# Kernel tuning notes

Hardware: AMD Instinct MI355X
Metric: run time of the kernel (lower is better)

Reference implementation:

```python
import jax, jax.numpy as jnp
import numpy as np

B, C, CI, H, W = 8, 1024, 512, 56, 56
BN_EPS = 1e-5


def _conv1x1(x, w, b):
    # x: [B,C,H,W], w: [O,C], b: [O] -> [B,O,H,W]
    return jnp.einsum('bchw,oc->bohw', x, w) + b[None, :, None, None]


def setup_inputs() -> dict:
    key = jax.random.key(0)
    ks = jax.random.split(key, 12)
    s = lambda k, shape: (jax.random.normal(k, shape, jnp.float32) * 0.02)
    return {
        'x': jax.random.normal(ks[0], (B, C, H, W), jnp.float32),
        'theta_w': s(ks[1], (CI, C)), 'theta_b': s(ks[2], (CI,)),
        'phi_w': s(ks[3], (CI, C)), 'phi_b': s(ks[4], (CI,)),
        'g_w': s(ks[5], (CI, C)), 'g_b': s(ks[6], (CI,)),
        'wz_w': s(ks[7], (C, CI)), 'wz_b': s(ks[8], (C,)),
        'bn_gamma': 1.0 + 0.1 * jax.random.normal(ks[9], (C,), jnp.float32),
        'bn_beta': s(ks[10], (C,)),
    }


def reference(x, theta_w, theta_b, phi_w, phi_b, g_w, g_b, wz_w, wz_b, bn_gamma, bn_beta):
    b, c, h, w = x.shape
    n = h * w
    # 1x1-conv projections, flattened to token sequences
    g_x = _conv1x1(x, g_w, g_b).reshape(b, -1, n).transpose(0, 2, 1)       # [B,N,CI]
    theta_x = _conv1x1(x, theta_w, theta_b).reshape(b, -1, n).transpose(0, 2, 1)  # [B,N,CI]
    phi_x = _conv1x1(x, phi_w, phi_b).reshape(b, -1, n)                     # [B,CI,N]
    # embedded-gaussian: f = theta @ phi^T, softmax over last dim
    f = jnp.einsum('bnc,bcm->bnm', theta_x, phi_x)                          # [B,N,N]
    attn = jax.nn.softmax(f, axis=-1)
    y = jnp.einsum('bnm,bmc->bnc', attn, g_x)                               # [B,N,CI]
    y = y.transpose(0, 2, 1).reshape(b, -1, h, w)                           # [B,CI,H,W]
    z = _conv1x1(y, wz_w, wz_b)                                             # [B,C,H,W]
    # BatchNorm2d in training mode: batch statistics over (B,H,W), biased var
    mean = z.mean(axis=(0, 2, 3))
    var = z.var(axis=(0, 2, 3))
    zn = (z - mean[None, :, None, None]) * jax.lax.rsqrt(var + BN_EPS)[None, :, None, None]
    zn = zn * bn_gamma[None, :, None, None] + bn_beta[None, :, None, None]
    return zn + x
```

## Files before the change

### kernel.cpp

```cpp
#include <hip/hip_runtime.h>
#include <cstdint>
#include <cstdio>

#define DEVINL __device__ __forceinline__

typedef _Float16 f16x8 __attribute__((ext_vector_type(8)));
typedef float    f32x4 __attribute__((ext_vector_type(4)));

static constexpr int B_  = 8;
static constexpr int C_  = 1024;
static constexpr int CI_ = 512;
static constexpr int N_  = 56 * 56;
static constexpr int NP  = 3328;
static constexpr float BN_EPS = 1e-5f;

DEVINL uint16_t f2h(float f) {
  union { _Float16 h; uint16_t u; } cv;
  cv.h = (_Float16)f;
  return cv.u;
}

DEVINL void async16(const void* g, void* lds) {
  __builtin_amdgcn_global_load_lds(
      (const __attribute__((address_space(1))) uint32_t*)g,
      (__attribute__((address_space(3))) uint32_t*)lds, 16, 0, 0);
}

template <int BIAS>
__global__ __launch_bounds__(512, 2) void gemm256(
    const uint16_t* __restrict__ A, const uint16_t* __restrict__ Bt,
    uint16_t* __restrict__ Cc, const float* __restrict__ bias,
    int K, int lda, int ldb, int ldc,
    long aBatch, long bBatch, long cBatch, int nbx, int nby) {
  __shared__ uint16_t lds[65536];

  const int nwg = gridDim.x, orig = blockIdx.x;
  const int q = nwg >> 3, r = nwg & 7, xcd = orig & 7, idx = orig >> 3;
  const int wgid = (xcd < r ? xcd * (q + 1) : r * (q + 1) + (xcd - r) * q) + idx;
  const int bx = wgid % nbx;
  const int by = (wgid / nbx) % nby;
  const int zb = wgid / (nbx * nby);

  const int tid = threadIdx.x, w = tid >> 6, l = tid & 63;
  const int wm = w >> 2, wn = w & 3, lr = l & 15, lg = l >> 4;

  const uint16_t* Ab = A + (long)zb * aBatch + (long)bx * 256 * lda;
  const uint16_t* Bb = Bt + (long)zb * bBatch + (long)by * 256 * ldb;

  const int NT = K >> 6;

  const int c0 = tid, c1 = 512 + tid;
  const long aoff0 = (long)(c0 >> 2) * lda + (((c0 & 3) ^ ((c0 >> 3) & 3)) * 8);
  const long aoff1 = (long)(c1 >> 2) * lda + (((c1 & 3) ^ ((c1 >> 3) & 3)) * 8);
  const long boff0 = (long)(c0 >> 2) * ldb + (((c0 & 3) ^ ((c0 >> 3) & 3)) * 8);
  const long boff1 = (long)(c1 >> 2) * ldb + (((c1 & 3) ^ ((c1 >> 3) & 3)) * 8);
  const int ldsW0 = (w * 64) * 8;
  const int ldsW1 = (512 + w * 64) * 8;

  auto stageA = [&](int t, int ks, int buf) {
    const int tw = t >= NT ? t - NT : t;
    const uint16_t* src = Ab + tw * 64 + ks * 32;
    const int reg = (buf * 2 + ks) * 8192;
    async16(src + aoff0, &lds[reg + ldsW0]);
    async16(src + aoff1, &lds[reg + ldsW1]);
  };
  auto stageB = [&](int t, int ks, int buf) {
    const int tw = t >= NT ? t - NT : t;
    const uint16_t* src = Bb + tw * 64 + ks * 32;
    const int reg = 32768 + (buf * 2 + ks) * 8192;
    async16(src + boff0, &lds[reg + ldsW0]);
    async16(src + boff1, &lds[reg + ldsW1]);
  };

  const int laneSwz = (lg ^ ((lr >> 1) & 3)) * 8;
  f32x4 acc[8][4] = {};
  f16x8 af[4], bf[4];

#define LOAD_A(b, ks, mh)                                                     \
  _Pragma("unroll") for (int i = 0; i < 4; ++i) {                             \
    const int row_ = wm * 128 + ((mh) * 4 + i) * 16 + lr;                     \
    af[i] = *reinterpret_cast<const f16x8*>(                                  \
        &lds[((b) * 2 + (ks)) * 8192 + row_ * 32 + laneSwz]);                 \
  }
#define LOAD_B(b, ks)                                                         \
  _Pragma("unroll") for (int i = 0; i < 4; ++i) {                             \
    const int row_ = wn * 64 + i * 16 + lr;                                   \
    bf[i] = *reinterpret_cast<const f16x8*>(                                  \
        &lds[32768 + ((b) * 2 + (ks)) * 8192 + row_ * 32 + laneSwz]);         \
  }
#define MFMA16(mh)                                                            \
  _Pragma("unroll") for (int i = 0; i < 4; ++i)                               \
  _Pragma("unroll") for (int j = 0; j < 4; ++j)                               \
    acc[(mh) * 4 + i][j] = __builtin_amdgcn_mfma_f32_16x16x32_f16(            \
        af[i], bf[j], acc[(mh) * 4 + i][j], 0, 0, 0);
#define WAIT_LGKM()                                       \
  asm volatile("s_waitcnt lgkmcnt(0)" ::: "memory");      \
  __builtin_amdgcn_sched_barrier(0);
#define WAIT_VM8()                                        \
  asm volatile("s_waitcnt vmcnt(8)" ::: "memory");        \
  __builtin_amdgcn_sched_barrier(0);

#define TILE(t, b)                                                            \
  {                                                                           \
                                                   \
    LOAD_B(b, 0); LOAD_A(b, 0, 0);                                            \
    stageA((t) + 1, 1, (b) ^ 1);                                              \
    __builtin_amdgcn_s_barrier(); WAIT_LGKM();                                \
    __builtin_amdgcn_s_setprio(1); MFMA16(0); __builtin_amdgcn_s_setprio(0);  \
    __builtin_amdgcn_s_barrier();                                             \
                                                   \
    LOAD_A(b, 0, 1);                                                          \
    stageB((t) + 1, 1, (b) ^ 1);                                              \
    __builtin_amdgcn_s_barrier(); WAIT_LGKM();                                \
    __builtin_amdgcn_s_setprio(1); MFMA16(1); __builtin_amdgcn_s_setprio(0);  \
    WAIT_VM8();                                                               \
    __builtin_amdgcn_s_barrier();                                             \
                                                   \
    LOAD_B(b, 1); LOAD_A(b, 1, 0);                                            \
    stageA((t) + 2, 0, (b));                                                  \
    __builtin_amdgcn_s_barrier(); WAIT_LGKM();                                \
    __builtin_amdgcn_s_setprio(1); MFMA16(0); __builtin_amdgcn_s_setprio(0);  \
    __builtin_amdgcn_s_barrier();                                             \
                                                   \
    LOAD_A(b, 1, 1);                                                          \
    stageB((t) + 2, 0, (b));                                                  \
    __builtin_amdgcn_s_barrier(); WAIT_LGKM();                                \
    __builtin_amdgcn_s_setprio(1); MFMA16(1); __builtin_amdgcn_s_setprio(0);  \
    WAIT_VM8();                                                               \
    __builtin_amdgcn_s_barrier();                                             \
  }

  stageA(0, 0, 0); stageB(0, 0, 0);
  stageA(0, 1, 0); stageB(0, 1, 0);
  stageA(1, 0, 1); stageB(1, 0, 1);
  WAIT_VM8();
  __builtin_amdgcn_s_barrier();

  for (int tp = 0; tp < NT; tp += 2) {
    TILE(tp, 0);
    TILE(tp + 1, 1);
  }

#undef TILE
#undef LOAD_A
#undef LOAD_B
#undef MFMA16
#undef WAIT_LGKM
#undef WAIT_VM8

  uint16_t* Cp = Cc + (long)zb * cBatch + ((long)bx * 256) * ldc + (long)by * 256;
#pragma unroll
  for (int mf = 0; mf < 8; ++mf) {
#pragma unroll
    for (int nf = 0; nf < 4; ++nf) {
      const int col = wn * 64 + nf * 16 + lr;
      const f32x4 v = acc[mf][nf];
#pragma unroll
      for (int qq = 0; qq < 4; ++qq) {
        const int row = wm * 128 + mf * 16 + lg * 4 + qq;
        float val = v[qq];
        if constexpr (BIAS == 1) val += bias[bx * 256 + row];
        if constexpr (BIAS == 2) val += bias[by * 256 + col];
        Cp[(long)row * ldc + col] = f2h(val);
      }
    }
  }
}

__global__ __launch_bounds__(256) void transpose_cast(
    const float* __restrict__ x, uint16_t* __restrict__ xT) {
  __shared__ float t[32][33];
  const int b = blockIdx.z;
  const float* xb = x + (long)b * C_ * N_;
  uint16_t* xTb = xT + (long)b * NP * C_;
  const int n0 = blockIdx.x * 32, c0 = blockIdx.y * 32;
  const int tx = threadIdx.x & 31, ty = threadIdx.x >> 5;
#pragma unroll
  for (int i = 0; i < 4; ++i) {
    const int cc = c0 + ty + i * 8, nn = n0 + tx;
    t[ty + i * 8][tx] = (nn < N_) ? xb[(long)cc * N_ + nn] : 0.f;
  }
  __syncthreads();
#pragma unroll
  for (int i = 0; i < 4; ++i) {
    const int nn = n0 + ty + i * 8, cc = c0 + tx;
    xTb[(long)nn * C_ + cc] = f2h(t[tx][ty + i * 8]);
  }
}

__global__ __launch_bounds__(256) void cvt_f16(
    const float* __restrict__ src, uint16_t* __restrict__ dst, int n) {
  int i = blockIdx.x * 256 + threadIdx.x;
  const int stride = gridDim.x * 256;
  for (; i < n; i += stride) dst[i] = f2h(src[i]);
}

__global__ __launch_bounds__(256) void concat_bias(
    const float* __restrict__ a, const float* __restrict__ b,
    float* __restrict__ d) {
  const int i = blockIdx.x * 256 + threadIdx.x;
  if (i < 512) d[i] = a[i];
  else if (i < 1024) d[i] = b[i - 512];
}

__global__ __launch_bounds__(256) void softmax_inplace(uint16_t* __restrict__ f) {
  const int row = blockIdx.x, tid = threadIdx.x;
  uint16_t* p = f + ((long)blockIdx.y * NP + row) * NP;
  if (row >= N_) {
    for (int i = tid; i < NP; i += 256) p[i] = 0;
    return;
  }
  __shared__ float buf[N_];
  __shared__ float red[8];
  float mx = -3.4e38f;
  for (int ch = tid; ch < N_ / 8; ch += 256) {
    const f16x8 v = *reinterpret_cast<const f16x8*>(p + ch * 8);
#pragma unroll
    for (int j = 0; j < 8; ++j) {
      const float fv = (float)v[j];
      buf[ch * 8 + j] = fv;
      mx = fmaxf(mx, fv);
    }
  }
  for (int o = 32; o; o >>= 1) mx = fmaxf(mx, __shfl_xor(mx, o));
  if ((tid & 63) == 0) red[tid >> 6] = mx;
  __syncthreads();
  mx = fmaxf(fmaxf(red[0], red[1]), fmaxf(red[2], red[3]));

  float s = 0.f;
  for (int i = tid; i < N_; i += 256) {
    const float e = __expf(buf[i] - mx);
    buf[i] = e;
    s += e;
  }
  for (int o = 32; o; o >>= 1) s += __shfl_xor(s, o);
  __syncthreads();
  if ((tid & 63) == 0) red[tid >> 6] = s;
  __syncthreads();
  const float rinv = 1.0f / (red[0] + red[1] + red[2] + red[3]);

  for (int ch = tid; ch < N_ / 8; ch += 256) {
    f16x8 o8;
#pragma unroll
    for (int j = 0; j < 8; ++j) o8[j] = (_Float16)(buf[ch * 8 + j] * rinv);
    *reinterpret_cast<f16x8*>(p + ch * 8) = o8;
  }
  for (int i = N_ + tid; i < NP; i += 256) p[i] = 0;
}

__global__ __launch_bounds__(256) void bn_stats(
    const _Float16* __restrict__ z, const float* __restrict__ gamma,
    const float* __restrict__ beta, float* __restrict__ ss) {
  const int c = blockIdx.x, tid = threadIdx.x;
  float sum = 0.f, sq = 0.f;
  for (int b = 0; b < B_; ++b) {
    const _Float16* zp = z + ((long)b * C_ + c) * NP;
    for (int ch = tid; ch < N_ / 8; ch += 256) {
      const f16x8 v = *(const f16x8*)(zp + ch * 8);
#pragma unroll
      for (int j = 0; j < 8; ++j) {
        const float fv = (float)v[j];
        sum += fv;
        sq += fv * fv;
      }
    }
  }
  for (int o = 32; o; o >>= 1) {
    sum += __shfl_xor(sum, o);
    sq += __shfl_xor(sq, o);
  }
  __shared__ float r1[8], r2[8];
  if ((tid & 63) == 0) { r1[tid >> 6] = sum; r2[tid >> 6] = sq; }
  __syncthreads();
  if (tid == 0) {
    sum = r1[0] + r1[1] + r1[2] + r1[3];
    sq  = r2[0] + r2[1] + r2[2] + r2[3];
    const float inv_n = 1.0f / (float)(B_ * N_);
    const float mean = sum * inv_n;
    const float var = sq * inv_n - mean * mean;
    const float sc = gamma[c] * rsqrtf(var + BN_EPS);
    ss[c] = sc;
    ss[C_ + c] = beta[c] - mean * sc;
  }
}

__global__ __launch_bounds__(256) void bn_apply(
    const _Float16* __restrict__ z, const float* __restrict__ x,
    const float* __restrict__ ss, float* __restrict__ out) {
  constexpr int CH = N_ / 8;
  const long nv = (long)B_ * C_ * CH;
  const long stride = (long)gridDim.x * 256;
  for (long v = (long)blockIdx.x * 256 + threadIdx.x; v < nv; v += stride) {
    const long row = v / CH;
    const int ch = (int)(v % CH);
    const int c = (int)(row % C_);
    const f16x8 zz = *(const f16x8*)(z + row * NP + ch * 8);
    const float4 x0 = *(const float4*)(x + row * (long)N_ + ch * 8);
    const float4 x1 = *(const float4*)(x + row * (long)N_ + ch * 8 + 4);
    const float sc = ss[c], sh = ss[C_ + c];
    float4 o0, o1;
    o0.x = (float)zz[0] * sc + sh + x0.x;
    o0.y = (float)zz[1] * sc + sh + x0.y;
    o0.z = (float)zz[2] * sc + sh + x0.z;
    o0.w = (float)zz[3] * sc + sh + x0.w;
    o1.x = (float)zz[4] * sc + sh + x1.x;
    o1.y = (float)zz[5] * sc + sh + x1.y;
    o1.z = (float)zz[6] * sc + sh + x1.z;
    o1.w = (float)zz[7] * sc + sh + x1.w;
    *(float4*)(out + row * (long)N_ + ch * 8) = o0;
    *(float4*)(out + row * (long)N_ + ch * 8 + 4) = o1;
  }
}

extern "C" void kernel_launch(void* const* d_in, const int* in_sizes, int n_in,
                              void* d_out, int out_size, void* d_ws,
                              size_t ws_size, hipStream_t stream) {
  const float* x       = (const float*)d_in[0];
  const float* theta_w = (const float*)d_in[1];
  const float* theta_b = (const float*)d_in[2];
  const float* phi_w   = (const float*)d_in[3];
  const float* phi_b   = (const float*)d_in[4];
  const float* g_w     = (const float*)d_in[5];
  const float* g_b     = (const float*)d_in[6];
  const float* wz_w    = (const float*)d_in[7];
  const float* wz_b    = (const float*)d_in[8];
  const float* gamma   = (const float*)d_in[9];
  const float* beta    = (const float*)d_in[10];
  float* out = (float*)d_out;

  char* ws = (char*)d_ws;
  size_t off = 0;
  auto alloc = [&](size_t bytes) {
    void* p = ws + off;
    off += (bytes + 255) & ~(size_t)255;
    return p;
  };
  uint16_t* wfused = (uint16_t*)alloc((size_t)1024 * 1024 * 2);
  uint16_t* wg     = (uint16_t*)alloc((size_t)CI_ * C_ * 2);
  uint16_t* wzh    = (uint16_t*)alloc((size_t)C_ * CI_ * 2);
  float*    bfused = (float*)alloc((size_t)1024 * 4);
  uint16_t* projT  = (uint16_t*)alloc((size_t)B_ * NP * 1024 * 2);
  uint16_t* gbuf   = (uint16_t*)alloc((size_t)B_ * CI_ * NP * 2);
  uint16_t* ybuf   = (uint16_t*)alloc((size_t)B_ * NP * CI_ * 2);
  uint16_t* zbuf   = (uint16_t*)alloc((size_t)B_ * C_ * NP * 2);
  float*    ss     = (float*)alloc((size_t)C_ * 2 * 4);

  const size_t xTb = (size_t)B_ * NP * C_ * 2;
  const size_t attnB = (size_t)NP * NP * 2;
  int G = 8;
  while (G > 1 && off + ((xTb > (size_t)G * attnB ? xTb : (size_t)G * attnB) + 255) > ws_size)
    G >>= 1;
  const size_t regionB = xTb > (size_t)G * attnB ? xTb : (size_t)G * attnB;
  uint16_t* xT    = (uint16_t*)alloc(regionB);
  uint16_t* fattn = xT;
  if (off > ws_size) {
    fprintf(stderr, "kernel_launch: workspace too small: need %zu have %zu\n",
            off, ws_size);
    return;
  }

  cvt_f16<<<512, 256, 0, stream>>>(theta_w, wfused, CI_ * C_);
  cvt_f16<<<512, 256, 0, stream>>>(phi_w, wfused + 512 * 1024, CI_ * C_);
  cvt_f16<<<512, 256, 0, stream>>>(g_w, wg, CI_ * C_);
  cvt_f16<<<512, 256, 0, stream>>>(wz_w, wzh, C_ * CI_);
  concat_bias<<<4, 256, 0, stream>>>(theta_b, phi_b, bfused);

  transpose_cast<<<dim3(NP / 32, C_ / 32, B_), 256, 0, stream>>>(x, xT);

  gemm256<2><<<dim3(B_ * NP / 256 * 4), 512, 0, stream>>>(
      xT, wfused, projT, bfused, C_, C_, C_, 1024,
      0, 0, 0, B_ * NP / 256, 4);
  gemm256<1><<<dim3(2 * 13 * B_), 512, 0, stream>>>(
      wg, xT, gbuf, g_b, C_, C_, C_, NP,
      0, (long)NP * C_, (long)CI_ * NP, 2, 13);

  for (int g0 = 0; g0 < B_; g0 += G) {
    gemm256<0><<<dim3(13 * 13 * G), 512, 0, stream>>>(
        projT + (size_t)g0 * NP * 1024, projT + (size_t)g0 * NP * 1024 + 512,
        fattn, nullptr, CI_, 1024, 1024, NP,
        (long)NP * 1024, (long)NP * 1024, (long)NP * NP, 13, 13);
    softmax_inplace<<<dim3(NP, G), 256, 0, stream>>>(fattn);
    gemm256<0><<<dim3(13 * 2 * G), 512, 0, stream>>>(
        fattn, gbuf + (size_t)g0 * CI_ * NP, ybuf + (size_t)g0 * NP * CI_,
        nullptr, NP, NP, NP, CI_,
        (long)NP * NP, (long)CI_ * NP, (long)NP * CI_, 13, 2);
  }
  gemm256<1><<<dim3(4 * 13 * B_), 512, 0, stream>>>(
      wzh, ybuf, zbuf, wz_b, CI_, CI_, CI_, NP,
      0, (long)NP * CI_, (long)C_ * NP, 4, 13);

  bn_stats<<<C_, 256, 0, stream>>>((const _Float16*)zbuf, gamma, beta, ss);
  bn_apply<<<4096, 256, 0, stream>>>((const _Float16*)zbuf, x, ss, out);
}
```

Before: 513.2 us.

## Fuse softmax statistics and BN statistics into GEMM epilogues, apply exp in PV GEMM

Removes the standalone softmax pass over the NxN attention matrix. The QK^T GEMM epilogue now emits per-tile row max and sum-exp partials, which a small combine kernel merges. The PV GEMM then exponentiates the raw logits in LDS before the MFMAs and scales its output by 1/sum. The BN statistics kernel is replaced by per-tile sum and sum-of-squares partials from the output GEMM epilogue. All batches are processed in one launch instead of groups, which needs a workspace of B*NP*NP. The change adds exp work and an extra barrier per K-substep inside the PV GEMM, and uses K=N_ with an odd-tile tail path. Padded columns (3136..3327) of f are not zeroed, so exp of those garbage values may enter the PV product unless the K truncation to N_ excludes them.

After: 581.9 us. +13.4%, slower.

```diff
diff --git a/kernel.cpp b/kernel.cpp
--- a/kernel.cpp
+++ b/kernel.cpp
@@ -26,12 +26,15 @@
       (__attribute__((address_space(3))) uint32_t*)lds, 16, 0, 0);
 }
 
-template <int BIAS>
+template <int BIAS, int RED, int EXPA>
 __global__ __launch_bounds__(512, 2) void gemm256(
     const uint16_t* __restrict__ A, const uint16_t* __restrict__ Bt,
     uint16_t* __restrict__ Cc, const float* __restrict__ bias,
     int K, int lda, int ldb, int ldc,
-    long aBatch, long bBatch, long cBatch, int nbx, int nby) {
+    long aBatch, long bBatch, long cBatch, int nbx, int nby,
+    const float* __restrict__ rowM, const float* __restrict__ rowScale,
+    long rmBatch, float* __restrict__ p0, float* __restrict__ p1,
+    int pstr, int nvalid) {
   __shared__ uint16_t lds[65536];
 
   const int nwg = gridDim.x, orig = blockIdx.x;
@@ -48,6 +51,15 @@
   const uint16_t* Bb = Bt + (long)zb * bBatch + (long)by * 256 * ldb;
 
   const int NT = K >> 6;
+
+  float mA0 = 0.f, mA1 = 0.f;
+  const float* rscB = nullptr;
+  if constexpr (EXPA) {
+    const float* rm = rowM + (long)zb * rmBatch + (long)bx * 256;
+    mA0 = rm[tid >> 2];
+    mA1 = rm[128 + (tid >> 2)];
+    rscB = rowScale + (long)zb * rmBatch + (long)bx * 256;
+  }
 
   const int c0 = tid, c1 = 512 + tid;
   const long aoff0 = (long)(c0 >> 2) * lda + (((c0 & 3) ^ ((c0 >> 3) & 3)) * 8);
@@ -58,14 +70,14 @@
   const int ldsW1 = (512 + w * 64) * 8;
 
   auto stageA = [&](int t, int ks, int buf) {
-    const int tw = t >= NT ? t - NT : t;
+    int tw = t; while (tw >= NT) tw -= NT;
     const uint16_t* src = Ab + tw * 64 + ks * 32;
     const int reg = (buf * 2 + ks) * 8192;
     async16(src + aoff0, &lds[reg + ldsW0]);
     async16(src + aoff1, &lds[reg + ldsW1]);
   };
   auto stageB = [&](int t, int ks, int buf) {
-    const int tw = t >= NT ? t - NT : t;
+    int tw = t; while (tw >= NT) tw -= NT;
     const uint16_t* src = Bb + tw * 64 + ks * 32;
     const int reg = 32768 + (buf * 2 + ks) * 8192;
     async16(src + boff0, &lds[reg + ldsW0]);
@@ -99,9 +111,26 @@
 #define WAIT_VM8()                                        \
   asm volatile("s_waitcnt vmcnt(8)" ::: "memory");        \
   __builtin_amdgcn_sched_barrier(0);
+#define PREP(b, ks)                                                           \
+  if constexpr (EXPA) {                                                       \
+    const int base_ = ((b) * 2 + (ks)) * 8192;                                \
+    f16x8 v0_ = *reinterpret_cast<const f16x8*>(&lds[base_ + tid * 8]);       \
+    f16x8 v1_ = *reinterpret_cast<const f16x8*>(&lds[base_ + (512 + tid) * 8]);\
+    f16x8 o0_, o1_;                                                           \
+    _Pragma("unroll") for (int j = 0; j < 8; ++j) {                           \
+      o0_[j] = (_Float16)__expf((float)v0_[j] - mA0);                         \
+      o1_[j] = (_Float16)__expf((float)v1_[j] - mA1);                         \
+    }                                                                         \
+    *reinterpret_cast<f16x8*>(&lds[base_ + tid * 8]) = o0_;                   \
+    *reinterpret_cast<f16x8*>(&lds[base_ + (512 + tid) * 8]) = o1_;           \
+    asm volatile("s_waitcnt lgkmcnt(0)" ::: "memory");                        \
+    __builtin_amdgcn_sched_barrier(0);                                        \
+    __builtin_amdgcn_s_barrier();                                             \
+  }
 
 #define TILE(t, b)                                                            \
   {                                                                           \
+    PREP(b, 0)                                                                \
                                                    \
     LOAD_B(b, 0); LOAD_A(b, 0, 0);                                            \
     stageA((t) + 1, 1, (b) ^ 1);                                              \
@@ -115,6 +144,7 @@
     __builtin_amdgcn_s_setprio(1); MFMA16(1); __builtin_amdgcn_s_setprio(0);  \
     WAIT_VM8();                                                               \
     __builtin_amdgcn_s_barrier();                                             \
+    PREP(b, 1)                                                                \
                                                    \
     LOAD_B(b, 1); LOAD_A(b, 1, 0);                                            \
     stageA((t) + 2, 0, (b));                                                  \
@@ -136,12 +166,15 @@
   WAIT_VM8();
   __builtin_amdgcn_s_barrier();
 
-  for (int tp = 0; tp < NT; tp += 2) {
+  const int NTE = NT & ~1;
+  for (int tp = 0; tp < NTE; tp += 2) {
     TILE(tp, 0);
     TILE(tp + 1, 1);
   }
+  if (NT & 1) TILE(NT - 1, 0);
 
 #undef TILE
+#undef PREP
 #undef LOAD_A
 #undef LOAD_B
 #undef MFMA16
@@ -161,8 +194,83 @@
         float val = v[qq];
         if constexpr (BIAS == 1) val += bias[bx * 256 + row];
         if constexpr (BIAS == 2) val += bias[by * 256 + col];
+        if constexpr (EXPA) val *= rscB[row];
         Cp[(long)row * ldc + col] = f2h(val);
       }
+    }
+  }
+
+  if constexpr (RED != 0) {
+    float* red = reinterpret_cast<float*>(lds);
+#pragma unroll
+    for (int mf = 0; mf < 8; ++mf) {
+#pragma unroll
+      for (int qq = 0; qq < 4; ++qq) {
+        float a_, b_;
+        if constexpr (RED == 1) {
+          float v[4];
+          float mx = -3.4e38f;
+#pragma unroll
+          for (int nf = 0; nf < 4; ++nf) {
+            const int colg = by * 256 + wn * 64 + nf * 16 + lr;
+            v[nf] = (colg < nvalid) ? acc[mf][nf][qq] : -3.4e38f;
+            mx = fmaxf(mx, v[nf]);
+          }
+          for (int k = 1; k < 16; k <<= 1) mx = fmaxf(mx, __shfl_xor(mx, k));
+          float se = 0.f;
+#pragma unroll
+          for (int nf = 0; nf < 4; ++nf) se += __expf(v[nf] - mx);
+          for (int k = 1; k < 16; k <<= 1) se += __shfl_xor(se, k);
+          a_ = mx; b_ = se;
+        } else {
+          const int row = wm * 128 + mf * 16 + lg * 4 + qq;
+          float bv = 0.f;
+          if constexpr (BIAS == 1) bv = bias[bx * 256 + row];
+          float s1 = 0.f, s2 = 0.f;
+#pragma unroll
+          for (int nf = 0; nf < 4; ++nf) {
+            const int colg = by * 256 + wn * 64 + nf * 16 + lr;
+            if (colg < nvalid) {
+              const float v = acc[mf][nf][qq] + bv;
+              s1 += v; s2 += v * v;
+            }
+          }
+          for (int k = 1; k < 16; k <<= 1) {
+            s1 += __shfl_xor(s1, k);
+            s2 += __shfl_xor(s2, k);
+          }
+          a_ = s1; b_ = s2;
+        }
+        if (lr == 0) {
+          const int row = wm * 128 + mf * 16 + lg * 4 + qq;
+          red[(row * 4 + wn) * 2 + 0] = a_;
+          red[(row * 4 + wn) * 2 + 1] = b_;
+        }
+      }
+    }
+    __syncthreads();
+    if (tid < 256) {
+      float r0[4], r1[4];
+#pragma unroll
+      for (int j = 0; j < 4; ++j) {
+        r0[j] = red[(tid * 4 + j) * 2 + 0];
+        r1[j] = red[(tid * 4 + j) * 2 + 1];
+      }
+      long prow; int pidx; float oa, ob;
+      if constexpr (RED == 1) {
+        const float M = fmaxf(fmaxf(r0[0], r0[1]), fmaxf(r0[2], r0[3]));
+        float S = 0.f;
+#pragma unroll
+        for (int j = 0; j < 4; ++j) S += r1[j] * __expf(r0[j] - M);
+        prow = ((long)zb * nbx + bx) * 256 + tid; pidx = by;
+        oa = M; ob = S;
+      } else {
+        oa = r0[0] + r0[1] + r0[2] + r0[3];
+        ob = r1[0] + r1[1] + r1[2] + r1[3];
+        prow = (long)bx * 256 + tid; pidx = zb * nby + by;
+      }
+      p0[prow * pstr + pidx] = oa;
+      p1[prow * pstr + pidx] = ob;
     }
   }
 }
@@ -203,85 +311,39 @@
   else if (i < 1024) d[i] = b[i - 512];
 }
 
-__global__ __launch_bounds__(256) void softmax_inplace(uint16_t* __restrict__ f) {
-  const int row = blockIdx.x, tid = threadIdx.x;
-  uint16_t* p = f + ((long)blockIdx.y * NP + row) * NP;
-  if (row >= N_) {
-    for (int i = tid; i < NP; i += 256) p[i] = 0;
-    return;
-  }
-  __shared__ float buf[N_];
-  __shared__ float red[8];
-  float mx = -3.4e38f;
-  for (int ch = tid; ch < N_ / 8; ch += 256) {
-    const f16x8 v = *reinterpret_cast<const f16x8*>(p + ch * 8);
-#pragma unroll
-    for (int j = 0; j < 8; ++j) {
-      const float fv = (float)v[j];
-      buf[ch * 8 + j] = fv;
-      mx = fmaxf(mx, fv);
-    }
-  }
-  for (int o = 32; o; o >>= 1) mx = fmaxf(mx, __shfl_xor(mx, o));
-  if ((tid & 63) == 0) red[tid >> 6] = mx;
-  __syncthreads();
-  mx = fmaxf(fmaxf(red[0], red[1]), fmaxf(red[2], red[3]));
-
-  float s = 0.f;
-  for (int i = tid; i < N_; i += 256) {
-    const float e = __expf(buf[i] - mx);
-    buf[i] = e;
-    s += e;
-  }
-  for (int o = 32; o; o >>= 1) s += __shfl_xor(s, o);
-  __syncthreads();
-  if ((tid & 63) == 0) red[tid >> 6] = s;
-  __syncthreads();
-  const float rinv = 1.0f / (red[0] + red[1] + red[2] + red[3]);
-
-  for (int ch = tid; ch < N_ / 8; ch += 256) {
-    f16x8 o8;
-#pragma unroll
-    for (int j = 0; j < 8; ++j) o8[j] = (_Float16)(buf[ch * 8 + j] * rinv);
-    *reinterpret_cast<f16x8*>(p + ch * 8) = o8;
-  }
-  for (int i = N_ + tid; i < NP; i += 256) p[i] = 0;
-}
-
-__global__ __launch_bounds__(256) void bn_stats(
-    const _Float16* __restrict__ z, const float* __restrict__ gamma,
-    const float* __restrict__ beta, float* __restrict__ ss) {
-  const int c = blockIdx.x, tid = threadIdx.x;
-  float sum = 0.f, sq = 0.f;
-  for (int b = 0; b < B_; ++b) {
-    const _Float16* zp = z + ((long)b * C_ + c) * NP;
-    for (int ch = tid; ch < N_ / 8; ch += 256) {
-      const f16x8 v = *(const f16x8*)(zp + ch * 8);
-#pragma unroll
-      for (int j = 0; j < 8; ++j) {
-        const float fv = (float)v[j];
-        sum += fv;
-        sq += fv * fv;
-      }
-    }
-  }
-  for (int o = 32; o; o >>= 1) {
-    sum += __shfl_xor(sum, o);
-    sq += __shfl_xor(sq, o);
-  }
-  __shared__ float r1[8], r2[8];
-  if ((tid & 63) == 0) { r1[tid >> 6] = sum; r2[tid >> 6] = sq; }
-  __syncthreads();
-  if (tid == 0) {
-    sum = r1[0] + r1[1] + r1[2] + r1[3];
-    sq  = r2[0] + r2[1] + r2[2] + r2[3];
-    const float inv_n = 1.0f / (float)(B_ * N_);
-    const float mean = sum * inv_n;
-    const float var = sq * inv_n - mean * mean;
-    const float sc = gamma[c] * rsqrtf(var + BN_EPS);
-    ss[c] = sc;
-    ss[C_ + c] = beta[c] - mean * sc;
-  }
+__global__ __launch_bounds__(256) void softmax_combine(
+    const float* __restrict__ pm, const float* __restrict__ ps,
+    float* __restrict__ rowM, float* __restrict__ rowScale) {
+  const int g = blockIdx.x * 256 + threadIdx.x;
+  if (g >= B_ * NP) return;
+  float M = -3.4e38f;
+#pragma unroll
+  for (int j = 0; j < 13; ++j) M = fmaxf(M, pm[(long)g * 13 + j]);
+  float S = 0.f;
+#pragma unroll
+  for (int j = 0; j < 13; ++j)
+    S += ps[(long)g * 13 + j] * __expf(pm[(long)g * 13 + j] - M);
+  rowM[g] = M;
+  rowScale[g] = 1.0f / S;
+}
+
+__global__ __launch_bounds__(256) void bn_finalize(
+    const float* __restrict__ pzs, const float* __restrict__ pzq,
+    const float* __restrict__ gamma, const float* __restrict__ beta,
+    float* __restrict__ ss) {
+  const int c = blockIdx.x * 256 + threadIdx.x;
+  if (c >= C_) return;
+  float s = 0.f, sq = 0.f;
+  for (int j = 0; j < 104; ++j) {
+    s += pzs[(long)c * 104 + j];
+    sq += pzq[(long)c * 104 + j];
+  }
+  const float inv_n = 1.0f / (float)(B_ * N_);
+  const float mean = s * inv_n;
+  const float var = sq * inv_n - mean * mean;
+  const float sc = gamma[c] * rsqrtf(var + BN_EPS);
+  ss[c] = sc;
+  ss[C_ + c] = beta[c] - mean * sc;
 }
 
 __global__ __launch_bounds__(256) void bn_apply(
@@ -344,14 +406,16 @@
   uint16_t* ybuf   = (uint16_t*)alloc((size_t)B_ * NP * CI_ * 2);
   uint16_t* zbuf   = (uint16_t*)alloc((size_t)B_ * C_ * NP * 2);
   float*    ss     = (float*)alloc((size_t)C_ * 2 * 4);
+  float*    pm     = (float*)alloc((size_t)B_ * NP * 13 * 4);
+  float*    ps     = (float*)alloc((size_t)B_ * NP * 13 * 4);
+  float*    rowM   = (float*)alloc((size_t)B_ * NP * 4);
+  float*    rowSc  = (float*)alloc((size_t)B_ * NP * 4);
+  float*    pzs    = (float*)alloc((size_t)C_ * 104 * 4);
+  float*    pzq    = (float*)alloc((size_t)C_ * 104 * 4);
 
   const size_t xTb = (size_t)B_ * NP * C_ * 2;
-  const size_t attnB = (size_t)NP * NP * 2;
-  int G = 8;
-  while (G > 1 && off + ((xTb > (size_t)G * attnB ? xTb : (size_t)G * attnB) + 255) > ws_size)
-    G >>= 1;
-  const size_t regionB = xTb > (size_t)G * attnB ? xTb : (size_t)G * attnB;
-  uint16_t* xT    = (uint16_t*)alloc(regionB);
+  const size_t fB  = (size_t)B_ * NP * NP * 2;
+  uint16_t* xT    = (uint16_t*)alloc(fB > xTb ? fB : xTb);
   uint16_t* fattn = xT;
   if (off > ws_size) {
     fprintf(stderr, "kernel_launch: workspace too small: need %zu have %zu\n",
@@ -367,28 +431,31 @@
 
   transpose_cast<<<dim3(NP / 32, C_ / 32, B_), 256, 0, stream>>>(x, xT);
 
-  gemm256<2><<<dim3(B_ * NP / 256 * 4), 512, 0, stream>>>(
+  gemm256<2, 0, 0><<<dim3(B_ * NP / 256 * 4), 512, 0, stream>>>(
       xT, wfused, projT, bfused, C_, C_, C_, 1024,
-      0, 0, 0, B_ * NP / 256, 4);
-  gemm256<1><<<dim3(2 * 13 * B_), 512, 0, stream>>>(
+      0, 0, 0, B_ * NP / 256, 4,
+      nullptr, nullptr, 0, nullptr, nullptr, 0, 0);
+  gemm256<1, 0, 0><<<dim3(2 * 13 * B_), 512, 0, stream>>>(
       wg, xT, gbuf, g_b, C_, C_, C_, NP,
-      0, (long)NP * C_, (long)CI_ * NP, 2, 13);
-
-  for (int g0 = 0; g0 < B_; g0 += G) {
-    gemm256<0><<<dim3(13 * 13 * G), 512, 0, stream>>>(
-        projT + (size_t)g0 * NP * 1024, projT + (size_t)g0 * NP * 1024 + 512,
-        fattn, nullptr, CI_, 1024, 1024, NP,
-        (long)NP * 1024, (long)NP * 1024, (long)NP * NP, 13, 13);
-    softmax_inplace<<<dim3(NP, G), 256, 0, stream>>>(fattn);
-    gemm256<0><<<dim3(13 * 2 * G), 512, 0, stream>>>(
-        fattn, gbuf + (size_t)g0 * CI_ * NP, ybuf + (size_t)g0 * NP * CI_,
-        nullptr, NP, NP, NP, CI_,
-        (long)NP * NP, (long)CI_ * NP, (long)NP * CI_, 13, 2);
-  }
-  gemm256<1><<<dim3(4 * 13 * B_), 512, 0, stream>>>(
+      0, (long)NP * C_, (long)CI_ * NP, 2, 13,
+      nullptr, nullptr, 0, nullptr, nullptr, 0, 0);
+
+  gemm256<0, 1, 0><<<dim3(13 * 13 * B_), 512, 0, stream>>>(
+      projT, projT + 512, fattn, nullptr, CI_, 1024, 1024, NP,
+      (long)NP * 1024, (long)NP * 1024, (long)NP * NP, 13, 13,
+      nullptr, nullptr, 0, pm, ps, 13, N_);
+  softmax_combine<<<dim3(B_ * NP / 256), 256, 0, stream>>>(pm, ps, rowM, rowSc);
+
+  gemm256<0, 0, 1><<<dim3(13 * 2 * B_), 512, 0, stream>>>(
+      fattn, gbuf, ybuf, nullptr, N_, NP, NP, CI_,
+      (long)NP * NP, (long)CI_ * NP, (long)NP * CI_, 13, 2,
+      rowM, rowSc, NP, nullptr, nullptr, 0, 0);
+
+  gemm256<1, 2, 0><<<dim3(4 * 13 * B_), 512, 0, stream>>>(
       wzh, ybuf, zbuf, wz_b, CI_, CI_, CI_, NP,
-      0, (long)NP * CI_, (long)C_ * NP, 4, 13);
-
-  bn_stats<<<C_, 256, 0, stream>>>((const _Float16*)zbuf, gamma, beta, ss);
+      0, (long)NP * CI_, (long)C_ * NP, 4, 13,
+      nullptr, nullptr, 0, pzs, pzq, 104, N_);
+
+  bn_finalize<<<dim3(4), 256, 0, stream>>>(pzs, pzq, gamma, beta, ss);
   bn_apply<<<4096, 256, 0, stream>>>((const _Float16*)zbuf, x, ss, out);
 }
```
